# Optimization experiments

Measured on AMD Instinct MI355X. Metric: run time of the kernel, lower is better.

The kernel has to match this reference:

```python
import jax, jax.numpy as jnp
import numpy as np

N = 100000
E = 600000
D_IN, D_HID, D_OUT = 128, 128, 64


def setup_inputs() -> dict:
    key = jax.random.key(0)
    k1, k2, k3, k4 = jax.random.split(key, 4)
    x = jax.random.normal(k1, (N, D_IN), dtype=jnp.float32)
    edge_index = jax.random.randint(k2, (2, E), 0, N, dtype=jnp.int64)
    edge_weight = jnp.ones((E,), dtype=jnp.float32)
    W1 = jax.random.normal(k3, (D_IN, D_HID), dtype=jnp.float32) / np.sqrt(D_IN)
    b1 = jnp.zeros((D_HID,), dtype=jnp.float32)
    W2 = jax.random.normal(k4, (D_HID, D_OUT), dtype=jnp.float32) / np.sqrt(D_HID)
    b2 = jnp.zeros((D_OUT,), dtype=jnp.float32)
    return {"x": x, "edge_index": edge_index, "edge_weight": edge_weight,
            "W1": W1, "b1": b1, "W2": W2, "b2": b2}


def _gcn_conv(x, row, col, ew, W, b, n_nodes):
    # x: [N, d_in]; row/col/ew include self loops. PyG gcn_norm:
    # deg[i] = sum of ew over edges with target i; norm = d^-1/2[row]*ew*d^-1/2[col]
    deg = jax.ops.segment_sum(ew, col, num_segments=n_nodes)
    dinv = jnp.where(deg > 0, jax.lax.rsqrt(deg), 0.0)
    norm = dinv[row] * ew * dinv[col]  # [E+N]
    xw = x @ W  # dense transform first (d_out <= d_in path)
    msg = xw[row] * norm[:, None]  # gather + scale  [E+N, d_out]
    out = jax.ops.segment_sum(msg, col, num_segments=n_nodes)  # scatter-add
    return out + b


def reference(x, edge_index, edge_weight, W1, b1, W2, b2):
    n = x.shape[0]
    loops = jnp.arange(n, dtype=edge_index.dtype)
    row = jnp.concatenate([edge_index[0], loops])
    col = jnp.concatenate([edge_index[1], loops])
    ew = jnp.concatenate([edge_weight, jnp.ones((n,), dtype=edge_weight.dtype)])
    # dropout is identity in eval mode
    h = jax.nn.relu(_gcn_conv(x, row, col, ew, W1, b1, n))
    out = _gcn_conv(h, row, col, ew, W2, b2, n)
    return out
```

## Files before the change

### kernel.cpp

```cpp
#include <hip/hip_runtime.h>


constexpr int SCAN_BLOCKS = 256;

typedef __attribute__((ext_vector_type(8))) short short8;
typedef __attribute__((ext_vector_type(4))) float f32x4;

__device__ __forceinline__ ushort f2bf(float f) {
    unsigned u = __float_as_uint(f);
    return (ushort)((u + 0x7fffu + ((u >> 16) & 1u)) >> 16);
}
__device__ __forceinline__ float bf2f(ushort h) {
    return __uint_as_float((unsigned)h << 16);
}

__global__ __launch_bounds__(256) void prep_kernel(
        int* __restrict__ cnt, int N,
        const float* __restrict__ W1, ushort* __restrict__ W1t,
        const float* __restrict__ W2, ushort* __restrict__ W2t) {
    const int n4c = (N + 3) >> 2;
    const int nbz = (n4c + 255) / 256;
    int b = blockIdx.x;
    if (b < nbz) {
        const int i = b * 256 + threadIdx.x;
        if (i < n4c) reinterpret_cast<int4*>(cnt)[i] = make_int4(0, 0, 0, 0);
        return;
    }
    b -= nbz;
    if (b < 64) {
        const int o = b * 256 + threadIdx.x;
        W1t[o] = f2bf(W1[(size_t)(o & 127) * 128 + (o >> 7)]);
        return;
    }
    b -= 64;
    {
        const int o = b * 256 + threadIdx.x;
        if (o < 64 * 128)
            W2t[o] = f2bf(W2[(size_t)(o & 127) * 64 + (o >> 7)]);
    }
}

__global__ __launch_bounds__(256, 2) void combo1_kernel(
        const float* __restrict__ X, const ushort* __restrict__ W1t,
        ushort* __restrict__ Ab, int N, int G,
        const int* __restrict__ col, int* __restrict__ cnt,
        int* __restrict__ rank, int E) {
    __shared__ __align__(16) ushort sX[128 * 128];
    __shared__ __align__(16) ushort sW[128 * 128];
    const int tid = threadIdx.x;

    if (blockIdx.x >= G) {
        const int T = (gridDim.x - G) * 256;
        for (int e = (blockIdx.x - G) * 256 + tid; e < E; e += T)
            rank[e] = atomicAdd(&cnt[col[e]], 1);
        return;
    }

    const int base = blockIdx.x * 128;
    #pragma unroll
    for (int p = 0; p < 8; p++) {
        const int ch = p * 256 + tid;
        const int r = ch >> 4, cpos = ch & 15;
        const int grow = base + r;
        uint4 u = make_uint4(0, 0, 0, 0);
        if (grow < N) {
            const float* xp = X + (size_t)grow * 128 + cpos * 8;
            const float4 a = *reinterpret_cast<const float4*>(xp);
            const float4 c = *reinterpret_cast<const float4*>(xp + 4);
            u.x = (uint)f2bf(a.x) | ((uint)f2bf(a.y) << 16);
            u.y = (uint)f2bf(a.z) | ((uint)f2bf(a.w) << 16);
            u.z = (uint)f2bf(c.x) | ((uint)f2bf(c.y) << 16);
            u.w = (uint)f2bf(c.z) | ((uint)f2bf(c.w) << 16);
        }
        const int b = (cpos * 16) ^ ((r & 7) << 4);
        *reinterpret_cast<uint4*>(reinterpret_cast<char*>(sX) + r * 256 + b) = u;
    }
    #pragma unroll
    for (int p = 0; p < 8; p++) {
        const int ch = p * 256 + tid;
        const int r = ch >> 4, cpos = ch & 15;
        uint4 v = *reinterpret_cast<const uint4*>(W1t + (size_t)r * 128 + cpos * 8);
        const int b = (cpos * 16) ^ ((r & 7) << 4);
        *reinterpret_cast<uint4*>(reinterpret_cast<char*>(sW) + r * 256 + b) = v;
    }
    __syncthreads();

    const int lane = tid & 63;
    const int wid = tid >> 6;
    const int wr = wid >> 1;
    const int wc = wid & 1;
    const int lr = lane & 15;
    const int g  = lane >> 4;

    f32x4 acc[4][4];
    #pragma unroll
    for (int i = 0; i < 4; i++)
        #pragma unroll
        for (int f = 0; f < 4; f++) acc[i][f] = (f32x4){0.f, 0.f, 0.f, 0.f};

    #pragma unroll
    for (int ks = 0; ks < 4; ks++) {
        const int koff = ks * 64 + g * 16;
        short8 a[4], b[4];
        #pragma unroll
        for (int i = 0; i < 4; i++) {
            const int row = wr * 64 + i * 16 + lr;
            a[i] = *reinterpret_cast<const short8*>(
                reinterpret_cast<const char*>(sX) + row * 256 + (koff ^ ((row & 7) << 4)));
        }
        #pragma unroll
        for (int f = 0; f < 4; f++) {
            const int c = wc * 64 + f * 16 + lr;
            b[f] = *reinterpret_cast<const short8*>(
                reinterpret_cast<const char*>(sW) + c * 256 + (koff ^ ((c & 7) << 4)));
        }
        #pragma unroll
        for (int i = 0; i < 4; i++)
            #pragma unroll
            for (int f = 0; f < 4; f++)
                acc[i][f] = __builtin_amdgcn_mfma_f32_16x16x32_bf16(a[i], b[f], acc[i][f], 0, 0, 0);
    }

    #pragma unroll
    for (int i = 0; i < 4; i++)
        #pragma unroll
        for (int reg = 0; reg < 4; reg++) {
            const int grow = base + wr * 64 + i * 16 + g * 4 + reg;
            if (grow < N)
                #pragma unroll
                for (int f = 0; f < 4; f++)
                    Ab[(size_t)grow * 128 + wc * 64 + f * 16 + lr] = f2bf(acc[i][f][reg]);
        }
}

__global__ __launch_bounds__(256) void scan_part_kernel(
        const int* __restrict__ cnt, int* __restrict__ partial, int N) {
    const int T = SCAN_BLOCKS * 256;
    const int chunk = (N + T - 1) / T;
    const int j = blockIdx.x * 256 + threadIdx.x;
    const int s = j * chunk, e = min(s + chunk, N);
    int acc = 0;
    for (int i = s; i < e; i++) acc += cnt[i];
    __shared__ int red[256];
    red[threadIdx.x] = acc;
    __syncthreads();
    for (int off = 128; off > 0; off >>= 1) {
        if (threadIdx.x < off) red[threadIdx.x] += red[threadIdx.x + off];
        __syncthreads();
    }
    if (threadIdx.x == 0) partial[blockIdx.x] = red[0];
}

__global__ __launch_bounds__(256) void scan_write_kernel(
        const int* __restrict__ cnt, const int* __restrict__ partial,
        int* __restrict__ rowptr, int N) {
    __shared__ int tp[256];
    __shared__ int sh[256];
    const int t = threadIdx.x;
    tp[t] = partial[t];
    __syncthreads();
    for (int off = 1; off < 256; off <<= 1) {
        int x = tp[t];
        int a = (t >= off) ? tp[t - off] : 0;
        __syncthreads();
        tp[t] = x + a;
        __syncthreads();
    }
    const int blockOff = (blockIdx.x == 0) ? 0 : tp[blockIdx.x - 1];

    const int T = SCAN_BLOCKS * 256;
    const int chunk = (N + T - 1) / T;
    const int j = blockIdx.x * 256 + t;
    const int s = j * chunk, e = min(s + chunk, N);
    int acc = 0;
    for (int i = s; i < e; i++) acc += cnt[i];
    sh[t] = acc;
    __syncthreads();
    for (int off = 1; off < 256; off <<= 1) {
        int x = sh[t];
        int a = (t >= off) ? sh[t - off] : 0;
        __syncthreads();
        sh[t] = x + a;
        __syncthreads();
    }
    int excl = blockOff + ((t == 0) ? 0 : sh[t - 1]);
    for (int i = s; i < e; i++) {
        rowptr[i] = excl;
        excl += cnt[i];
    }
    if (j == T - 1) rowptr[N] = excl;
}

__global__ void fill_kernel(const int* __restrict__ row, const int* __restrict__ col,
        const float* __restrict__ ew, const int* __restrict__ rowptr,
        const int* __restrict__ rank, int2* __restrict__ csr, int E) {
    int e = blockIdx.x * blockDim.x + threadIdx.x;
    if (e < E) {
        const int p = rowptr[col[e]] + rank[e];
        csr[p] = make_int2(row[e], __float_as_int(ew[e]));
    }
}

__global__ __launch_bounds__(256) void degsum_kernel(
        const int* __restrict__ rowptr, const int2* __restrict__ csr,
        float* __restrict__ dinv, int N) {
    const int n = blockIdx.x * blockDim.x + threadIdx.x;
    if (n >= N) return;
    const int e0 = rowptr[n], e1 = rowptr[n + 1];
    float d = 1.0f;
    for (int e = e0; e < e1; e++) d += __int_as_float(csr[e].y);
    dinv[n] = (d > 0.0f) ? rsqrtf(d) : 0.0f;
}

__global__ __launch_bounds__(256) void agg1_kernel(
        const int* __restrict__ rowptr, const int2* __restrict__ csr,
        const float* __restrict__ dinv,
        const ushort* __restrict__ src, const float* __restrict__ bias,
        ushort* __restrict__ dst, int N) {
    const long long gid = (long long)blockIdx.x * blockDim.x + threadIdx.x;
    const int c = (int)(gid >> 4);
    if (c >= N) return;
    const int lane = (int)(gid & 15);
    const float di = dinv[c];
    const float sl = di * di;
    float acc[8];
    {
        const short8 s8 = *reinterpret_cast<const short8*>(src + (size_t)c * 128 + lane * 8);
        #pragma unroll
        for (int j = 0; j < 8; j++) acc[j] = bf2f((ushort)s8[j]) * sl;
    }
    const int e0 = rowptr[c], e1 = rowptr[c + 1];
    int e = e0;
    for (; e + 4 <= e1; e += 4) {
        const int2 c0 = csr[e], c1 = csr[e + 1], c2 = csr[e + 2], c3 = csr[e + 3];
        const float w0 = __int_as_float(c0.y) * dinv[c0.x] * di;
        const float w1 = __int_as_float(c1.y) * dinv[c1.x] * di;
        const float w2 = __int_as_float(c2.y) * dinv[c2.x] * di;
        const float w3 = __int_as_float(c3.y) * dinv[c3.x] * di;
        const short8 v0 = *reinterpret_cast<const short8*>(src + (size_t)c0.x * 128 + lane * 8);
        const short8 v1 = *reinterpret_cast<const short8*>(src + (size_t)c1.x * 128 + lane * 8);
        const short8 v2 = *reinterpret_cast<const short8*>(src + (size_t)c2.x * 128 + lane * 8);
        const short8 v3 = *reinterpret_cast<const short8*>(src + (size_t)c3.x * 128 + lane * 8);
        #pragma unroll
        for (int j = 0; j < 8; j++)
            acc[j] += bf2f((ushort)v0[j]) * w0 + bf2f((ushort)v1[j]) * w1 +
                      bf2f((ushort)v2[j]) * w2 + bf2f((ushort)v3[j]) * w3;
    }
    for (; e < e1; e++) {
        const int2 ce = csr[e];
        const float w = __int_as_float(ce.y) * dinv[ce.x] * di;
        const short8 v = *reinterpret_cast<const short8*>(src + (size_t)ce.x * 128 + lane * 8);
        #pragma unroll
        for (int j = 0; j < 8; j++) acc[j] += bf2f((ushort)v[j]) * w;
    }
    const float4 b0 = reinterpret_cast<const float4*>(bias)[lane * 2];
    const float4 b1 = reinterpret_cast<const float4*>(bias)[lane * 2 + 1];
    acc[0] = fmaxf(acc[0] + b0.x, 0.f); acc[1] = fmaxf(acc[1] + b0.y, 0.f);
    acc[2] = fmaxf(acc[2] + b0.z, 0.f); acc[3] = fmaxf(acc[3] + b0.w, 0.f);
    acc[4] = fmaxf(acc[4] + b1.x, 0.f); acc[5] = fmaxf(acc[5] + b1.y, 0.f);
    acc[6] = fmaxf(acc[6] + b1.z, 0.f); acc[7] = fmaxf(acc[7] + b1.w, 0.f);
    uint4 o;
    o.x = (uint)f2bf(acc[0]) | ((uint)f2bf(acc[1]) << 16);
    o.y = (uint)f2bf(acc[2]) | ((uint)f2bf(acc[3]) << 16);
    o.z = (uint)f2bf(acc[4]) | ((uint)f2bf(acc[5]) << 16);
    o.w = (uint)f2bf(acc[6]) | ((uint)f2bf(acc[7]) << 16);
    *reinterpret_cast<uint4*>(dst + (size_t)c * 128 + lane * 8) = o;
}

__global__ __launch_bounds__(256) void agg2_kernel(
        const int* __restrict__ rowptr, const int2* __restrict__ csr,
        const float* __restrict__ dinv,
        const ushort* __restrict__ src, const float* __restrict__ bias,
        float* __restrict__ dst, int N) {
    const long long gid = (long long)blockIdx.x * blockDim.x + threadIdx.x;
    const int c = (int)(gid >> 3);
    if (c >= N) return;
    const int lane = (int)(gid & 7);
    const float di = dinv[c];
    const float sl = di * di;
    float acc[8];
    {
        const short8 s8 = *reinterpret_cast<const short8*>(src + (size_t)c * 64 + lane * 8);
        #pragma unroll
        for (int j = 0; j < 8; j++) acc[j] = bf2f((ushort)s8[j]) * sl;
    }
    const int e0 = rowptr[c], e1 = rowptr[c + 1];
    int e = e0;
    for (; e + 4 <= e1; e += 4) {
        const int2 c0 = csr[e], c1 = csr[e + 1], c2 = csr[e + 2], c3 = csr[e + 3];
        const float w0 = __int_as_float(c0.y) * dinv[c0.x] * di;
        const float w1 = __int_as_float(c1.y) * dinv[c1.x] * di;
        const float w2 = __int_as_float(c2.y) * dinv[c2.x] * di;
        const float w3 = __int_as_float(c3.y) * dinv[c3.x] * di;
        const short8 v0 = *reinterpret_cast<const short8*>(src + (size_t)c0.x * 64 + lane * 8);
        const short8 v1 = *reinterpret_cast<const short8*>(src + (size_t)c1.x * 64 + lane * 8);
        const short8 v2 = *reinterpret_cast<const short8*>(src + (size_t)c2.x * 64 + lane * 8);
        const short8 v3 = *reinterpret_cast<const short8*>(src + (size_t)c3.x * 64 + lane * 8);
        #pragma unroll
        for (int j = 0; j < 8; j++)
            acc[j] += bf2f((ushort)v0[j]) * w0 + bf2f((ushort)v1[j]) * w1 +
                      bf2f((ushort)v2[j]) * w2 + bf2f((ushort)v3[j]) * w3;
    }
    for (; e < e1; e++) {
        const int2 ce = csr[e];
        const float w = __int_as_float(ce.y) * dinv[ce.x] * di;
        const short8 v = *reinterpret_cast<const short8*>(src + (size_t)ce.x * 64 + lane * 8);
        #pragma unroll
        for (int j = 0; j < 8; j++) acc[j] += bf2f((ushort)v[j]) * w;
    }
    const float4 b0 = reinterpret_cast<const float4*>(bias)[lane * 2];
    const float4 b1 = reinterpret_cast<const float4*>(bias)[lane * 2 + 1];
    float* dp = dst + (size_t)c * 64 + lane * 8;
    *reinterpret_cast<float4*>(dp) =
        make_float4(acc[0] + b0.x, acc[1] + b0.y, acc[2] + b0.z, acc[3] + b0.w);
    *reinterpret_cast<float4*>(dp + 4) =
        make_float4(acc[4] + b1.x, acc[5] + b1.y, acc[6] + b1.z, acc[7] + b1.w);
}

__global__ __launch_bounds__(256, 2) void gemm2_kernel(
        const ushort* __restrict__ Xb, const ushort* __restrict__ Wt,
        ushort* __restrict__ Y, int N) {
    __shared__ __align__(16) ushort sX[128 * 128];
    __shared__ __align__(16) ushort sW[64 * 128];
    const int tid = threadIdx.x;
    const int base = blockIdx.x * 128;

    #pragma unroll
    for (int p = 0; p < 8; p++) {
        const int ch = p * 256 + tid;
        const int r = ch >> 4, cpos = ch & 15;
        const int grow = base + r;
        uint4 v = make_uint4(0, 0, 0, 0);
        if (grow < N)
            v = *reinterpret_cast<const uint4*>(Xb + (size_t)grow * 128 + cpos * 8);
        const int b = (cpos * 16) ^ ((r & 7) << 4);
        *reinterpret_cast<uint4*>(reinterpret_cast<char*>(sX) + r * 256 + b) = v;
    }
    #pragma unroll
    for (int p = 0; p < 4; p++) {
        const int ch = p * 256 + tid;
        const int r = ch >> 4, cpos = ch & 15;
        uint4 v = *reinterpret_cast<const uint4*>(Wt + (size_t)r * 128 + cpos * 8);
        const int b = (cpos * 16) ^ ((r & 7) << 4);
        *reinterpret_cast<uint4*>(reinterpret_cast<char*>(sW) + r * 256 + b) = v;
    }
    __syncthreads();

    const int lane = tid & 63;
    const int wid = tid >> 6;
    const int lr = lane & 15;
    const int g  = lane >> 4;

    f32x4 acc[2][4];
    #pragma unroll
    for (int i = 0; i < 2; i++)
        #pragma unroll
        for (int f = 0; f < 4; f++) acc[i][f] = (f32x4){0.f, 0.f, 0.f, 0.f};

    #pragma unroll
    for (int ks = 0; ks < 4; ks++) {
        const int koff = ks * 64 + g * 16;
        short8 a[2], b[4];
        #pragma unroll
        for (int i = 0; i < 2; i++) {
            const int row = wid * 32 + i * 16 + lr;
            a[i] = *reinterpret_cast<const short8*>(
                reinterpret_cast<const char*>(sX) + row * 256 + (koff ^ ((row & 7) << 4)));
        }
        #pragma unroll
        for (int f = 0; f < 4; f++) {
            const int c = f * 16 + lr;
            b[f] = *reinterpret_cast<const short8*>(
                reinterpret_cast<const char*>(sW) + c * 256 + (koff ^ ((c & 7) << 4)));
        }
        #pragma unroll
        for (int i = 0; i < 2; i++)
            #pragma unroll
            for (int f = 0; f < 4; f++)
                acc[i][f] = __builtin_amdgcn_mfma_f32_16x16x32_bf16(a[i], b[f], acc[i][f], 0, 0, 0);
    }

    #pragma unroll
    for (int i = 0; i < 2; i++)
        #pragma unroll
        for (int reg = 0; reg < 4; reg++) {
            const int grow = base + wid * 32 + i * 16 + g * 4 + reg;
            if (grow < N)
                #pragma unroll
                for (int f = 0; f < 4; f++)
                    Y[(size_t)grow * 64 + f * 16 + lr] = f2bf(acc[i][f][reg]);
        }
}

extern "C" void kernel_launch(void* const* d_in, const int* in_sizes, int n_in,
                              void* d_out, int out_size, void* d_ws, size_t ws_size,
                              hipStream_t stream) {
    const float* x  = (const float*)d_in[0];
    const int*   ei = (const int*)d_in[1];
    const float* ew = (const float*)d_in[2];
    const float* W1 = (const float*)d_in[3];
    const float* b1 = (const float*)d_in[4];
    const float* W2 = (const float*)d_in[5];
    const float* b2 = (const float*)d_in[6];
    const int N = in_sizes[0] / 128;
    const int E = in_sizes[1] / 2;
    const int* row = ei;
    const int* col = ei + E;

    char* w = (char*)d_ws;
    float* dinv = (float*)w;                 w += (size_t)N * 4;
    ushort* Ab  = (ushort*)w;                w += (size_t)N * 256;
    ushort* Hb  = (ushort*)w;                w += (size_t)N * 256;
    ushort* Gb  = (ushort*)w;                w += (size_t)N * 128;
    ushort* W1t = (ushort*)w;                w += 128 * 128 * 2;
    ushort* W2t = (ushort*)w;                w += 64 * 128 * 2;
    int* cnt    = (int*)w;                   w += (size_t)N * 4 + 16;
    int* rowptr = (int*)w;                   w += (size_t)(N + 1) * 4;
    int* partial= (int*)w;                   w += SCAN_BLOCKS * 4;
    int* rank   = (int*)w;                   w += (size_t)E * 4;
    int2* csr   = (int2*)w;
    float* out  = (float*)d_out;

    const int ntiles = (N + 127) / 128;
    const int nbz = (((N + 3) >> 2) + 255) / 256;

    prep_kernel<<<nbz + 64 + 32, 256, 0, stream>>>(cnt, N, W1, W1t, W2, W2t);

    const int cntb = (E / 4 + 255) / 256;
    combo1_kernel<<<ntiles + cntb, 256, 0, stream>>>(x, W1t, Ab, N, ntiles,
                                                     col, cnt, rank, E);

    scan_part_kernel<<<SCAN_BLOCKS, 256, 0, stream>>>(cnt, partial, N);
    scan_write_kernel<<<SCAN_BLOCKS, 256, 0, stream>>>(cnt, partial, rowptr, N);
    fill_kernel<<<(E + 255) / 256, 256, 0, stream>>>(row, col, ew, rowptr, rank, csr, E);
    degsum_kernel<<<(N + 255) / 256, 256, 0, stream>>>(rowptr, csr, dinv, N);

    agg1_kernel<<<(int)(((long long)N * 16 + 255) / 256), 256, 0, stream>>>(
        rowptr, csr, dinv, Ab, b1, Hb, N);

    gemm2_kernel<<<ntiles, 256, 0, stream>>>(Hb, W2t, Gb, N);
    agg2_kernel<<<(int)(((long long)N * 8 + 255) / 256), 256, 0, stream>>>(
        rowptr, csr, dinv, Gb, b2, out, N);
}
```

Measured before the change: 131.0 us.

## Fold weight conversion and count zeroing into GEMM1, split edge counting out

Removes the separate prep kernel. GEMM1 now reads fp32 W1 directly and converts and transposes it into shared memory, while extra blocks zero the count array and convert W2. Edge counting with atomics moves to its own kernel after GEMM1, which fixes the ordering between zeroing and counting that the fused launch could not guarantee. Each GEMM1 block now does strided fp32 loads of W1, and one more launch is added back.

```diff
diff --git a/kernel.cpp b/kernel.cpp
--- a/kernel.cpp
+++ b/kernel.cpp
@@ -14,45 +14,27 @@
     return __uint_as_float((unsigned)h << 16);
 }
 
-__global__ __launch_bounds__(256) void prep_kernel(
-        int* __restrict__ cnt, int N,
-        const float* __restrict__ W1, ushort* __restrict__ W1t,
-        const float* __restrict__ W2, ushort* __restrict__ W2t) {
-    const int n4c = (N + 3) >> 2;
-    const int nbz = (n4c + 255) / 256;
-    int b = blockIdx.x;
-    if (b < nbz) {
-        const int i = b * 256 + threadIdx.x;
-        if (i < n4c) reinterpret_cast<int4*>(cnt)[i] = make_int4(0, 0, 0, 0);
-        return;
-    }
-    b -= nbz;
-    if (b < 64) {
-        const int o = b * 256 + threadIdx.x;
-        W1t[o] = f2bf(W1[(size_t)(o & 127) * 128 + (o >> 7)]);
-        return;
-    }
-    b -= 64;
-    {
-        const int o = b * 256 + threadIdx.x;
-        if (o < 64 * 128)
-            W2t[o] = f2bf(W2[(size_t)(o & 127) * 64 + (o >> 7)]);
-    }
-}
-
-__global__ __launch_bounds__(256, 2) void combo1_kernel(
-        const float* __restrict__ X, const ushort* __restrict__ W1t,
+__global__ __launch_bounds__(256, 2) void gemm1_kernel(
+        const float* __restrict__ X, const float* __restrict__ W1,
         ushort* __restrict__ Ab, int N, int G,
-        const int* __restrict__ col, int* __restrict__ cnt,
-        int* __restrict__ rank, int E) {
+        int* __restrict__ cnt, const float* __restrict__ W2,
+        ushort* __restrict__ W2t) {
     __shared__ __align__(16) ushort sX[128 * 128];
     __shared__ __align__(16) ushort sW[128 * 128];
     const int tid = threadIdx.x;
 
     if (blockIdx.x >= G) {
-        const int T = (gridDim.x - G) * 256;
-        for (int e = (blockIdx.x - G) * 256 + tid; e < E; e += T)
-            rank[e] = atomicAdd(&cnt[col[e]], 1);
+        const int b = blockIdx.x - G;
+        const int n4 = (N + 3) >> 2;
+        const int nbz = (n4 + 255) / 256;
+        if (b < nbz) {
+            const int i = b * 256 + tid;
+            if (i < n4) reinterpret_cast<int4*>(cnt)[i] = make_int4(0, 0, 0, 0);
+        } else {
+            const int o = (b - nbz) * 256 + tid;
+            if (o < 64 * 128)
+                W2t[o] = f2bf(W2[(size_t)(o & 127) * 64 + (o >> 7)]);
+        }
         return;
     }
 
@@ -78,10 +60,18 @@
     #pragma unroll
     for (int p = 0; p < 8; p++) {
         const int ch = p * 256 + tid;
-        const int r = ch >> 4, cpos = ch & 15;
-        uint4 v = *reinterpret_cast<const uint4*>(W1t + (size_t)r * 128 + cpos * 8);
-        const int b = (cpos * 16) ^ ((r & 7) << 4);
-        *reinterpret_cast<uint4*>(reinterpret_cast<char*>(sW) + r * 256 + b) = v;
+        const int c = ch & 127, kc = ch >> 7;
+        const int k0 = kc * 8;
+        float f[8];
+        #pragma unroll
+        for (int j = 0; j < 8; j++) f[j] = W1[(size_t)(k0 + j) * 128 + c];
+        uint4 u;
+        u.x = (uint)f2bf(f[0]) | ((uint)f2bf(f[1]) << 16);
+        u.y = (uint)f2bf(f[2]) | ((uint)f2bf(f[3]) << 16);
+        u.z = (uint)f2bf(f[4]) | ((uint)f2bf(f[5]) << 16);
+        u.w = (uint)f2bf(f[6]) | ((uint)f2bf(f[7]) << 16);
+        const int b = (k0 * 2) ^ ((c & 7) << 4);
+        *reinterpret_cast<uint4*>(reinterpret_cast<char*>(sW) + c * 256 + b) = u;
     }
     __syncthreads();
 
@@ -104,9 +94,9 @@
         short8 a[4], b[4];
         #pragma unroll
         for (int i = 0; i < 4; i++) {
-            const int row = wr * 64 + i * 16 + lr;
+            const int r = wr * 64 + i * 16 + lr;
             a[i] = *reinterpret_cast<const short8*>(
-                reinterpret_cast<const char*>(sX) + row * 256 + (koff ^ ((row & 7) << 4)));
+                reinterpret_cast<const char*>(sX) + r * 256 + (koff ^ ((r & 7) << 4)));
         }
         #pragma unroll
         for (int f = 0; f < 4; f++) {
@@ -131,6 +121,13 @@
                 for (int f = 0; f < 4; f++)
                     Ab[(size_t)grow * 128 + wc * 64 + f * 16 + lr] = f2bf(acc[i][f][reg]);
         }
+}
+
+__global__ void cnt_kernel(const int* __restrict__ col, int* __restrict__ cnt,
+                           int* __restrict__ rank, int E) {
+    const int T = gridDim.x * blockDim.x;
+    for (int e = blockIdx.x * blockDim.x + threadIdx.x; e < E; e += T)
+        rank[e] = atomicAdd(&cnt[col[e]], 1);
 }
 
 __global__ __launch_bounds__(256) void scan_part_kernel(
@@ -153,7 +150,7 @@
 
 __global__ __launch_bounds__(256) void scan_write_kernel(
         const int* __restrict__ cnt, const int* __restrict__ partial,
-        int* __restrict__ rowptr, int N) {
+        int* __restrict__ rowptr, int N, int E) {
     __shared__ int tp[256];
     __shared__ int sh[256];
     const int t = threadIdx.x;
@@ -167,7 +164,6 @@
         __syncthreads();
     }
     const int blockOff = (blockIdx.x == 0) ? 0 : tp[blockIdx.x - 1];
-
     const int T = SCAN_BLOCKS * 256;
     const int chunk = (N + T - 1) / T;
     const int j = blockIdx.x * 256 + t;
@@ -184,11 +180,8 @@
         __syncthreads();
     }
     int excl = blockOff + ((t == 0) ? 0 : sh[t - 1]);
-    for (int i = s; i < e; i++) {
-        rowptr[i] = excl;
-        excl += cnt[i];
-    }
-    if (j == T - 1) rowptr[N] = excl;
+    for (int i = s; i < e; i++) { rowptr[i] = excl; excl += cnt[i]; }
+    if (j == 0) rowptr[N] = E;
 }
 
 __global__ void fill_kernel(const int* __restrict__ row, const int* __restrict__ col,
@@ -217,10 +210,10 @@
         const float* __restrict__ dinv,
         const ushort* __restrict__ src, const float* __restrict__ bias,
         ushort* __restrict__ dst, int N) {
-    const long long gid = (long long)blockIdx.x * blockDim.x + threadIdx.x;
-    const int c = (int)(gid >> 4);
+    const int gid = blockIdx.x * 256 + threadIdx.x;
+    const int c = gid >> 4;
     if (c >= N) return;
-    const int lane = (int)(gid & 15);
+    const int lane = gid & 15;
     const float di = dinv[c];
     const float sl = di * di;
     float acc[8];
@@ -267,15 +260,90 @@
     *reinterpret_cast<uint4*>(dst + (size_t)c * 128 + lane * 8) = o;
 }
 
+__global__ __launch_bounds__(256, 2) void gemm2_kernel(
+        const ushort* __restrict__ Xb, const ushort* __restrict__ Wt,
+        ushort* __restrict__ Y, int N) {
+    __shared__ __align__(16) ushort sX[128 * 128];
+    __shared__ __align__(16) ushort sW[64 * 128];
+    const int tid = threadIdx.x;
+    const int base = blockIdx.x * 128;
+
+    #pragma unroll
+    for (int p = 0; p < 8; p++) {
+        const int ch = p * 256 + tid;
+        const int r = ch >> 4, cpos = ch & 15;
+        const int grow = base + r;
+        uint4 v = make_uint4(0, 0, 0, 0);
+        if (grow < N)
+            v = *reinterpret_cast<const uint4*>(Xb + (size_t)grow * 128 + cpos * 8);
+        const int b = (cpos * 16) ^ ((r & 7) << 4);
+        *reinterpret_cast<uint4*>(reinterpret_cast<char*>(sX) + r * 256 + b) = v;
+    }
+    #pragma unroll
+    for (int p = 0; p < 4; p++) {
+        const int ch = p * 256 + tid;
+        const int r = ch >> 4, cpos = ch & 15;
+        uint4 v = *reinterpret_cast<const uint4*>(Wt + (size_t)r * 128 + cpos * 8);
+        const int b = (cpos * 16) ^ ((r & 7) << 4);
+        *reinterpret_cast<uint4*>(reinterpret_cast<char*>(sW) + r * 256 + b) = v;
+    }
+    __syncthreads();
+
+    const int lane = tid & 63;
+    const int wid = tid >> 6;
+    const int lr = lane & 15;
+    const int g  = lane >> 4;
+
+    f32x4 acc[2][4];
+    #pragma unroll
+    for (int i = 0; i < 2; i++)
+        #pragma unroll
+        for (int f = 0; f < 4; f++) acc[i][f] = (f32x4){0.f, 0.f, 0.f, 0.f};
+
+    #pragma unroll
+    for (int ks = 0; ks < 4; ks++) {
+        const int koff = ks * 64 + g * 16;
+        short8 a[2], b[4];
+        #pragma unroll
+        for (int i = 0; i < 2; i++) {
+            const int r = wid * 32 + i * 16 + lr;
+            a[i] = *reinterpret_cast<const short8*>(
+                reinterpret_cast<const char*>(sX) + r * 256 + (koff ^ ((r & 7) << 4)));
+        }
+        #pragma unroll
+        for (int f = 0; f < 4; f++) {
+            const int c = f * 16 + lr;
+            b[f] = *reinterpret_cast<const short8*>(
+                reinterpret_cast<const char*>(sW) + c * 256 + (koff ^ ((c & 7) << 4)));
+        }
+        #pragma unroll
+        for (int i = 0; i < 2; i++)
+            #pragma unroll
+            for (int f = 0; f < 4; f++)
+                acc[i][f] = __builtin_amdgcn_mfma_f32_16x16x32_bf16(a[i], b[f], acc[i][f], 0, 0, 0);
+    }
+
+    #pragma unroll
+    for (int i = 0; i < 2; i++)
+        #pragma unroll
+        for (int reg = 0; reg < 4; reg++) {
+            const int grow = base + wid * 32 + i * 16 + g * 4 + reg;
+            if (grow < N)
+                #pragma unroll
+                for (int f = 0; f < 4; f++)
+                    Y[(size_t)grow * 64 + f * 16 + lr] = f2bf(acc[i][f][reg]);
+        }
+}
+
 __global__ __launch_bounds__(256) void agg2_kernel(
         const int* __restrict__ rowptr, const int2* __restrict__ csr,
         const float* __restrict__ dinv,
         const ushort* __restrict__ src, const float* __restrict__ bias,
         float* __restrict__ dst, int N) {
-    const long long gid = (long long)blockIdx.x * blockDim.x + threadIdx.x;
-    const int c = (int)(gid >> 3);
+    const int gid = blockIdx.x * 256 + threadIdx.x;
+    const int c = gid >> 3;
     if (c >= N) return;
-    const int lane = (int)(gid & 7);
+    const int lane = gid & 7;
     const float di = dinv[c];
     const float sl = di * di;
     float acc[8];
@@ -315,81 +383,6 @@
         make_float4(acc[0] + b0.x, acc[1] + b0.y, acc[2] + b0.z, acc[3] + b0.w);
     *reinterpret_cast<float4*>(dp + 4) =
         make_float4(acc[4] + b1.x, acc[5] + b1.y, acc[6] + b1.z, acc[7] + b1.w);
-}
-
-__global__ __launch_bounds__(256, 2) void gemm2_kernel(
-        const ushort* __restrict__ Xb, const ushort* __restrict__ Wt,
-        ushort* __restrict__ Y, int N) {
-    __shared__ __align__(16) ushort sX[128 * 128];
-    __shared__ __align__(16) ushort sW[64 * 128];
-    const int tid = threadIdx.x;
-    const int base = blockIdx.x * 128;
-
-    #pragma unroll
-    for (int p = 0; p < 8; p++) {
-        const int ch = p * 256 + tid;
-        const int r = ch >> 4, cpos = ch & 15;
-        const int grow = base + r;
-        uint4 v = make_uint4(0, 0, 0, 0);
-        if (grow < N)
-            v = *reinterpret_cast<const uint4*>(Xb + (size_t)grow * 128 + cpos * 8);
-        const int b = (cpos * 16) ^ ((r & 7) << 4);
-        *reinterpret_cast<uint4*>(reinterpret_cast<char*>(sX) + r * 256 + b) = v;
-    }
-    #pragma unroll
-    for (int p = 0; p < 4; p++) {
-        const int ch = p * 256 + tid;
-        const int r = ch >> 4, cpos = ch & 15;
-        uint4 v = *reinterpret_cast<const uint4*>(Wt + (size_t)r * 128 + cpos * 8);
-        const int b = (cpos * 16) ^ ((r & 7) << 4);
-        *reinterpret_cast<uint4*>(reinterpret_cast<char*>(sW) + r * 256 + b) = v;
-    }
-    __syncthreads();
-
-    const int lane = tid & 63;
-    const int wid = tid >> 6;
-    const int lr = lane & 15;
-    const int g  = lane >> 4;
-
-    f32x4 acc[2][4];
-    #pragma unroll
-    for (int i = 0; i < 2; i++)
-        #pragma unroll
-        for (int f = 0; f < 4; f++) acc[i][f] = (f32x4){0.f, 0.f, 0.f, 0.f};
-
-    #pragma unroll
-    for (int ks = 0; ks < 4; ks++) {
-        const int koff = ks * 64 + g * 16;
-        short8 a[2], b[4];
-        #pragma unroll
-        for (int i = 0; i < 2; i++) {
-            const int row = wid * 32 + i * 16 + lr;
-            a[i] = *reinterpret_cast<const short8*>(
-                reinterpret_cast<const char*>(sX) + row * 256 + (koff ^ ((row & 7) << 4)));
-        }
-        #pragma unroll
-        for (int f = 0; f < 4; f++) {
-            const int c = f * 16 + lr;
-            b[f] = *reinterpret_cast<const short8*>(
-                reinterpret_cast<const char*>(sW) + c * 256 + (koff ^ ((c & 7) << 4)));
-        }
-        #pragma unroll
-        for (int i = 0; i < 2; i++)
-            #pragma unroll
-            for (int f = 0; f < 4; f++)
-                acc[i][f] = __builtin_amdgcn_mfma_f32_16x16x32_bf16(a[i], b[f], acc[i][f], 0, 0, 0);
-    }
-
-    #pragma unroll
-    for (int i = 0; i < 2; i++)
-        #pragma unroll
-        for (int reg = 0; reg < 4; reg++) {
-            const int grow = base + wid * 32 + i * 16 + g * 4 + reg;
-            if (grow < N)
-                #pragma unroll
-                for (int f = 0; f < 4; f++)
-                    Y[(size_t)grow * 64 + f * 16 + lr] = f2bf(acc[i][f][reg]);
-        }
 }
 
 extern "C" void kernel_launch(void* const* d_in, const int* in_sizes, int n_in,
@@ -412,11 +405,10 @@
     ushort* Ab  = (ushort*)w;                w += (size_t)N * 256;
     ushort* Hb  = (ushort*)w;                w += (size_t)N * 256;
     ushort* Gb  = (ushort*)w;                w += (size_t)N * 128;
-    ushort* W1t = (ushort*)w;                w += 128 * 128 * 2;
     ushort* W2t = (ushort*)w;                w += 64 * 128 * 2;
     int* cnt    = (int*)w;                   w += (size_t)N * 4 + 16;
-    int* rowptr = (int*)w;                   w += (size_t)(N + 1) * 4;
-    int* partial= (int*)w;                   w += SCAN_BLOCKS * 4;
+    int* rowptr = (int*)w;                   w += (size_t)(N + 8) * 4;
+    int* partial= (int*)w;                   w += 2048 * 4;
     int* rank   = (int*)w;                   w += (size_t)E * 4;
     int2* csr   = (int2*)w;
     float* out  = (float*)d_out;
@@ -424,21 +416,14 @@
     const int ntiles = (N + 127) / 128;
     const int nbz = (((N + 3) >> 2) + 255) / 256;
 
-    prep_kernel<<<nbz + 64 + 32, 256, 0, stream>>>(cnt, N, W1, W1t, W2, W2t);
-
-    const int cntb = (E / 4 + 255) / 256;
-    combo1_kernel<<<ntiles + cntb, 256, 0, stream>>>(x, W1t, Ab, N, ntiles,
-                                                     col, cnt, rank, E);
-
+    gemm1_kernel<<<ntiles + nbz + 32, 256, 0, stream>>>(x, W1, Ab, N, ntiles,
+                                                        cnt, W2, W2t);
+    cnt_kernel<<<(E / 8 + 255) / 256, 256, 0, stream>>>(col, cnt, rank, E);
     scan_part_kernel<<<SCAN_BLOCKS, 256, 0, stream>>>(cnt, partial, N);
-    scan_write_kernel<<<SCAN_BLOCKS, 256, 0, stream>>>(cnt, partial, rowptr, N);
+    scan_write_kernel<<<SCAN_BLOCKS, 256, 0, stream>>>(cnt, partial, rowptr, N, E);
     fill_kernel<<<(E + 255) / 256, 256, 0, stream>>>(row, col, ew, rowptr, rank, csr, E);
     degsum_kernel<<<(N + 255) / 256, 256, 0, stream>>>(rowptr, csr, dinv, N);
-
-    agg1_kernel<<<(int)(((long long)N * 16 + 255) / 256), 256, 0, stream>>>(
-        rowptr, csr, dinv, Ab, b1, Hb, N);
-
+    agg1_kernel<<<(N * 16 + 255) / 256, 256, 0, stream>>>(rowptr, csr, dinv, Ab, b1, Hb, N);
     gemm2_kernel<<<ntiles, 256, 0, stream>>>(Hb, W2t, Gb, N);
-    agg2_kernel<<<(int)(((long long)N * 8 + 255) / 256), 256, 0, stream>>>(
-        rowptr, csr, dinv, Gb, b2, out, N);
-}
+    agg2_kernel<<<(N * 8 + 255) / 256, 256, 0, stream>>>(rowptr, csr, dinv, Gb, b2, out, N);
+}
```

Measured after the change: 135.6 us. +3.5%, slower.
